# Kernel optimization log

Measured on AMD Instinct MI355X. Metric: run time of the kernel, lower is better.

The kernel has to match this reference:

```python
import jax, jax.numpy as jnp
from jax import lax
import numpy as np

B, H, W = 2048, 28, 28
LATENT_EACH = 64
LATENT = 2 * LATENT_EACH  # 128
MEM_SIZE = 8192
TOPK = 10
EPS = 1e-12


def _conv(x, w, b):
    # x: NCHW, w: OIHW, 3x3 conv, padding=1 (SAME)
    y = lax.conv_general_dilated(x, w, (1, 1), 'SAME',
                                 dimension_numbers=('NCHW', 'OIHW', 'NCHW'))
    return y + b[None, :, None, None]


def _deconv(x, w, b):
    # ConvTranspose2d(k=4, stride=2, padding=1) -> out = 2*in (SAME transpose)
    # w: HWIO = (4,4,in,out)
    y = lax.conv_transpose(x, w, (2, 2), 'SAME',
                           dimension_numbers=('NCHW', 'HWIO', 'NCHW'))
    return y + b[None, :, None, None]


def _encoder(x, w1, b1, w2, b2, fcw, fcb):
    h = jax.nn.relu(_conv(x, w1, b1))
    h = jax.nn.relu(_conv(h, w2, b2))
    feat = h.mean(axis=(2, 3))  # AdaptiveAvgPool2d((1,1)) + flatten -> [B,64]
    return feat @ fcw.T + fcb


def _memory_match(z, mem):
    mn = mem / jnp.maximum(jnp.linalg.norm(mem, axis=1, keepdims=True), EPS)
    zn = z / jnp.maximum(jnp.linalg.norm(z, axis=1, keepdims=True), EPS)
    sim = zn @ mn.T                      # [B, MEM_SIZE]
    topv, topi = lax.top_k(sim, TOPK)    # [B, K]
    wts = jax.nn.softmax(topv, axis=1)   # [B, K]
    sel = mem[topi]                      # gather: [B, K, LATENT]
    return jnp.einsum('bk,bkd->bd', wts, sel)


def setup_inputs() -> dict:
    key = jax.random.key(0)
    ks = jax.random.split(key, 24)
    g = lambda k, s, scale=0.05: jax.random.normal(k, s, jnp.float32) * scale
    inp = {
        'x': jax.random.normal(ks[0], (B, 1, H, W), jnp.float32),
        # center encoder
        'ce_w1': g(ks[1], (32, 1, 3, 3)), 'ce_b1': jnp.zeros((32,), jnp.float32),
        'ce_w2': g(ks[2], (64, 32, 3, 3)), 'ce_b2': jnp.zeros((64,), jnp.float32),
        'ce_fcw': g(ks[3], (LATENT_EACH, 64)), 'ce_fcb': jnp.zeros((LATENT_EACH,), jnp.float32),
        # global encoder
        'ge_w1': g(ks[4], (32, 1, 3, 3)), 'ge_b1': jnp.zeros((32,), jnp.float32),
        'ge_w2': g(ks[5], (64, 32, 3, 3)), 'ge_b2': jnp.zeros((64,), jnp.float32),
        'ge_fcw': g(ks[6], (LATENT_EACH, 64)), 'ge_fcb': jnp.zeros((LATENT_EACH,), jnp.float32),
        # memory bank (Parameter ~ randn)
        'mem': jax.random.normal(ks[7], (MEM_SIZE, LATENT), jnp.float32),
        # decoder
        'dec_fcw': g(ks[8], (64 * 7 * 7, LATENT)), 'dec_fcb': jnp.zeros((64 * 7 * 7,), jnp.float32),
        'd_w1': g(ks[9], (4, 4, 64, 32)), 'd_b1': jnp.zeros((32,), jnp.float32),   # deconv 64->32
        'd_w2': g(ks[10], (16, 32, 3, 3)), 'd_b2': jnp.zeros((16,), jnp.float32),  # conv 32->16
        'd_w3': g(ks[11], (4, 4, 16, 8)), 'd_b3': jnp.zeros((8,), jnp.float32),    # deconv 16->8
        'd_w4': g(ks[12], (1, 8, 3, 3)), 'd_b4': jnp.zeros((1,), jnp.float32),     # conv 8->1
    }
    return inp


def reference(x, ce_w1, ce_b1, ce_w2, ce_b2, ce_fcw, ce_fcb,
              ge_w1, ge_b1, ge_w2, ge_b2, ge_fcw, ge_fcb,
              mem, dec_fcw, dec_fcb,
              d_w1, d_b1, d_w2, d_b2, d_w3, d_b3, d_w4, d_b4):
    # crop_center(x, 14): start = (28-14)//2 = 7
    x_center = x[:, :, 7:21, 7:21]
    z_center = _encoder(x_center, ce_w1, ce_b1, ce_w2, ce_b2, ce_fcw, ce_fcb)
    z_global = _encoder(x, ge_w1, ge_b1, ge_w2, ge_b2, ge_fcw, ge_fcb)
    z = jnp.concatenate([z_center, z_global], axis=1)  # [B, 128]
    z_match = _memory_match(z, mem)                    # [B, 128]
    d = (z_match @ dec_fcw.T + dec_fcb).reshape(B, 64, 7, 7)
    d = jax.nn.relu(_deconv(d, d_w1, d_b1))   # [B,32,14,14]
    d = jax.nn.relu(_conv(d, d_w2, d_b2))     # [B,16,14,14]
    d = jax.nn.relu(_deconv(d, d_w3, d_b3))   # [B,8,28,28]
    x_hat = _conv(d, d_w4, d_b4)              # [B,1,28,28]
    return x_hat
```

## Files before the change

kernel.cpp:

```cpp
#include <hip/hip_runtime.h>
#include <cfloat>
#include <cmath>

#define TPB 256

typedef _Float16 half8 __attribute__((ext_vector_type(8)));
typedef float floatx16 __attribute__((ext_vector_type(16)));
typedef float floatx4 __attribute__((ext_vector_type(4)));

__device__ __forceinline__ float wave_reduce_sum(float v) {
#pragma unroll
  for (int off = 32; off > 0; off >>= 1) v += __shfl_xor(v, off, 64);
  return v;
}

__global__ __launch_bounds__(64) void prep_bfrags(
    const float* __restrict__ ce_w2, const float* __restrict__ ge_w2,
    float* __restrict__ frags) {
  const int blk = blockIdx.x;
  const int enc = blk / 72;
  const int frag = blk % 72;
  const int ks = frag >> 2, part = (frag >> 1) & 1, nt = frag & 1;
  const int tap = ks >> 1, half = ks & 1;
  const int lane = threadIdx.x;
  const float* w2 = enc ? ge_w2 : ce_w2;
  const int n = nt * 32 + (lane & 31);
  const int cb = half * 16 + (lane >> 5) * 8;
  half8 out;
#pragma unroll
  for (int j = 0; j < 8; ++j) {
    float v = w2[(n * 32 + cb + j) * 9 + tap];
    _Float16 h = (_Float16)v;
    out[j] = (part == 0) ? h : (_Float16)((v - (float)h) * 4096.f);
  }
  *(half8*)((char*)frags + ((size_t)blk * 64 + lane) * 16) = out;
}

__global__ __launch_bounds__(64) void prep_dec1(
    const float* __restrict__ w1, float* __restrict__ frags) {
  const int blk = blockIdx.x;
  const int phase = blk >> 4, ks = blk & 15;
  const int pa = phase >> 1, pb = phase & 1;
  const int st = ks >> 2, kk = ks & 3;
  const int s = st >> 1, tt = st & 1;
  const int lane = threadIdx.x;
  const int kg = lane >> 5, n = lane & 31;
  const int tap = (pa + 2 * s) * 4 + (pb + 2 * tt);
  half8 o;
#pragma unroll
  for (int j = 0; j < 8; ++j) {
    int c = kk * 16 + kg * 8 + j;
    o[j] = (_Float16)w1[tap * 2048 + c * 32 + n];
  }
  *(half8*)((char*)frags + ((size_t)blk * 64 + lane) * 16) = o;
}

__global__ __launch_bounds__(64) void prep_dfc(
    const float* __restrict__ dfcw, float* __restrict__ frags) {
  const int blk = blockIdx.x;
  const int nt = blk >> 3, ks = blk & 7;
  const int lane = threadIdx.x;
  const int n = lane & 31, kg = lane >> 5;
  const int j = nt * 32 + n;
  const int px = j >> 6, c = j & 63;
  half8 o;
#pragma unroll
  for (int u = 0; u < 8; ++u)
    o[u] = (_Float16)dfcw[(size_t)(c * 49 + px) * 128 + ks * 16 + kg * 8 + u];
  *(half8*)((char*)frags + ((size_t)blk * 64 + lane) * 16) = o;
}

__global__ __launch_bounds__(64) void prep_mem(
    const float* __restrict__ memg, float* __restrict__ frags) {
  const int blk = blockIdx.x;
  const int slot = blk & 15;
  const int p = slot >> 3, ks = slot & 7;
  const int T = blk >> 4;
  const int lane = threadIdx.x;
  const int n = lane & 31, kg = lane >> 5;
  const float* src = memg + (size_t)(T * 32 + n) * 128 + ks * 16 + kg * 8;
  half8 o;
#pragma unroll
  for (int j = 0; j < 8; ++j) {
    float v = src[j];
    _Float16 h = (_Float16)v;
    o[j] = p ? (_Float16)((v - (float)h) * 4096.f) : h;
  }
  *(half8*)((char*)frags + ((size_t)blk * 64 + lane) * 16) = o;
}

__global__ __launch_bounds__(256) void norm_kernel(
    const float* __restrict__ memg, float* __restrict__ invn) {
  const int wv = threadIdx.x >> 6, lane = threadIdx.x & 63;
  const int row = blockIdx.x * 4 + wv;
  const float* r = memg + (size_t)row * 128;
  float a = r[lane], b = r[lane + 64];
  float s = wave_reduce_sum(a * a + b * b);
  if (lane == 0) invn[row] = 1.f / fmaxf(sqrtf(s), 1e-12f);
}

template <int S, bool CENTER>
__device__ __forceinline__ void encoder_body(
    char* smem, const float* __restrict__ x, const float* __restrict__ w1,
    const float* __restrict__ b1, const float* __restrict__ b2,
    const float* __restrict__ fcw, const float* __restrict__ fcb,
    const float* __restrict__ bfrag, float* __restrict__ zout, int zoff,
    int b) {
  constexpr int SP = S + 2;
  constexpr int NBANDS = (S == 28) ? 3 : 2;
  constexpr int RMAX = 12;
  constexpr int NPIX = RMAX * SP;
  constexpr int GSTB = NPIX * 16;
  constexpr int PSTB = 4 * GSTB;

  char* h1s = smem;
  float* xs = (float*)(smem + 2 * PSTB);
  float* w1s = xs + SP * SP;
  float(*featp)[64] = (float(*)[64])(w1s + 288);

  const int t = threadIdx.x;
  const int lane = t & 63;
  const int wv = t >> 6;

  for (int e = t; e < SP * SP; e += TPB) xs[e] = 0.f;
  for (int e = t; e < 288; e += TPB) w1s[e] = w1[e];
  __syncthreads();
  const float* xb = x + (size_t)b * 784 + (CENTER ? (7 * 28 + 7) : 0);
  for (int e = t; e < S * S; e += TPB) {
    int i = e / S, j = e - i * S;
    xs[(i + 1) * SP + (j + 1)] = xb[i * 28 + j];
  }

  float sp0 = 0.f, sp1 = 0.f;
  const float bias0 = b2[lane & 31];
  const float bias1 = b2[32 + (lane & 31)];
  const int gOff = (lane >> 5) * GSTB;
  const char* bgbase = (const char*)bfrag + lane * 16;

#pragma unroll
  for (int band = 0; band < NBANDS; ++band) {
    const int BH_ = (S == 28) ? ((band < 2) ? 10 : 8) : ((band == 0) ? 10 : 4);
    const int b0 = band * 10;
    const int LIMIT = BH_ * S;
    const int MTB = (LIMIT + 31) / 32;
    const int NBLK2 = (MTB + 1) / 2;

    __syncthreads();
    for (int e = t; e < 4 * NPIX; e += TPB) {
      int g = e / NPIX;
      int pix = e - g * NPIX;
      int lr = pix / SP;
      int cw = pix - lr * SP;
      int gr = b0 - 1 + lr;
      int ebase = g * GSTB + pix * 16;
      half8 hi8 = {}, lo8 = {};
      if (gr >= 0 && gr < S && cw >= 1 && cw <= S) {
        float xv[9];
#pragma unroll
        for (int di = 0; di < 3; ++di)
#pragma unroll
          for (int dj = 0; dj < 3; ++dj)
            xv[di * 3 + dj] = xs[(gr + di) * SP + (cw - 1 + dj)];
#pragma unroll
        for (int u = 0; u < 8; ++u) {
          int ch = g * 8 + u;
          float a = b1[ch];
#pragma unroll
          for (int v = 0; v < 9; ++v) a += xv[v] * w1s[ch * 9 + v];
          a = fmaxf(a, 0.f);
          _Float16 h = (_Float16)a;
          hi8[u] = h;
          lo8[u] = (_Float16)((a - (float)h) * 4096.f);
        }
      }
      *(half8*)(h1s + ebase) = hi8;
      *(half8*)(h1s + PSTB + ebase) = lo8;
    }
    __syncthreads();
    for (int mblk = wv; mblk < NBLK2; mblk += 4) {
      const int Mt0 = mblk * 2;
      floatx16 acc[2][2][2] = {};
      int pixB[2];
#pragma unroll
      for (int im = 0; im < 2; ++im) {
        int px = (Mt0 + im) * 32 + (lane & 31);
        px = px < LIMIT ? px : LIMIT - 1;
        int r = px / S;
        int cc = px - r * S;
        pixB[im] = (r * SP + cc) * 16;
      }
#pragma unroll 3
      for (int tap = 0; tap < 9; ++tap) {
        const int di = tap / 3, dj = tap - di * 3;
        const int offT = (di * SP + dj) * 16;
#pragma unroll
        for (int half = 0; half < 2; ++half) {
          const int ks = tap * 2 + half;
          const char* bp = bgbase + ks * 4096;
          const int offA = offT + gOff + half * (2 * GSTB);
          half8 ah0 = *(const half8*)(h1s + pixB[0] + offA);
          half8 al0 = *(const half8*)(h1s + PSTB + pixB[0] + offA);
          half8 ah1 = *(const half8*)(h1s + pixB[1] + offA);
          half8 al1 = *(const half8*)(h1s + PSTB + pixB[1] + offA);
          {
            half8 bh = *(const half8*)(bp);
            half8 bl = *(const half8*)(bp + 2048);
            acc[0][0][0] = __builtin_amdgcn_mfma_f32_32x32x16_f16(
                ah0, bh, acc[0][0][0], 0, 0, 0);
            acc[0][0][1] = __builtin_amdgcn_mfma_f32_32x32x16_f16(
                ah0, bl, acc[0][0][1], 0, 0, 0);
            acc[0][0][1] = __builtin_amdgcn_mfma_f32_32x32x16_f16(
                al0, bh, acc[0][0][1], 0, 0, 0);
            acc[1][0][0] = __builtin_amdgcn_mfma_f32_32x32x16_f16(
                ah1, bh, acc[1][0][0], 0, 0, 0);
            acc[1][0][1] = __builtin_amdgcn_mfma_f32_32x32x16_f16(
                ah1, bl, acc[1][0][1], 0, 0, 0);
            acc[1][0][1] = __builtin_amdgcn_mfma_f32_32x32x16_f16(
                al1, bh, acc[1][0][1], 0, 0, 0);
          }
          {
            half8 bh = *(const half8*)(bp + 1024);
            half8 bl = *(const half8*)(bp + 3072);
            acc[0][1][0] = __builtin_amdgcn_mfma_f32_32x32x16_f16(
                ah0, bh, acc[0][1][0], 0, 0, 0);
            acc[0][1][1] = __builtin_amdgcn_mfma_f32_32x32x16_f16(
                ah0, bl, acc[0][1][1], 0, 0, 0);
            acc[0][1][1] = __builtin_amdgcn_mfma_f32_32x32x16_f16(
                al0, bh, acc[0][1][1], 0, 0, 0);
            acc[1][1][0] = __builtin_amdgcn_mfma_f32_32x32x16_f16(
                ah1, bh, acc[1][1][0], 0, 0, 0);
            acc[1][1][1] = __builtin_amdgcn_mfma_f32_32x32x16_f16(
                ah1, bl, acc[1][1][1], 0, 0, 0);
            acc[1][1][1] = __builtin_amdgcn_mfma_f32_32x32x16_f16(
                al1, bh, acc[1][1][1], 0, 0, 0);
          }
        }
      }
#pragma unroll
      for (int im = 0; im < 2; ++im)
#pragma unroll
        for (int reg = 0; reg < 16; ++reg) {
          int row = (reg & 3) + 8 * (reg >> 2) + 4 * (lane >> 5);
          int p = (Mt0 + im) * 32 + row;
          if (p < LIMIT) {
            float v0 =
                acc[im][0][0][reg] + acc[im][0][1][reg] * (1.f / 4096.f) + bias0;
            float v1 =
                acc[im][1][0][reg] + acc[im][1][1][reg] * (1.f / 4096.f) + bias1;
            sp0 += fmaxf(v0, 0.f);
            sp1 += fmaxf(v1, 0.f);
          }
        }
    }
  }
  sp0 += __shfl_xor(sp0, 32);
  sp1 += __shfl_xor(sp1, 32);
  if (lane < 32) {
    featp[wv][lane] = sp0;
    featp[wv][32 + lane] = sp1;
  }
  __syncthreads();
  if (t < 64)
    featp[0][t] = (featp[0][t] + featp[1][t] + featp[2][t] + featp[3][t]) *
                  (1.f / (S * S));
  __syncthreads();
  if (t < 64) {
    float s = 0.f;
#pragma unroll
    for (int i = 0; i < 64; ++i) s += featp[0][i] * fcw[t * 64 + i];
    zout[(size_t)b * 128 + zoff + t] = s + fcb[t];
  }
}

__global__ __launch_bounds__(256, 3) void encoders_fused(
    const float* __restrict__ x, const float* __restrict__ ce_w1,
    const float* __restrict__ ce_b1, const float* __restrict__ ce_b2,
    const float* __restrict__ ce_fcw, const float* __restrict__ ce_fcb,
    const float* __restrict__ ge_w1, const float* __restrict__ ge_b1,
    const float* __restrict__ ge_b2, const float* __restrict__ ge_fcw,
    const float* __restrict__ ge_fcb, const float* __restrict__ frags,
    float* __restrict__ z) {
  __shared__ __align__(16) char smem[51856];
  if (blockIdx.x < 2048)
    encoder_body<28, false>(smem, x, ge_w1, ge_b1, ge_b2, ge_fcw, ge_fcb,
                            frags + 18432, z, 64, blockIdx.x);
  else
    encoder_body<14, true>(smem, x, ce_w1, ce_b1, ce_b2, ce_fcw, ce_fcb, frags,
                           z, 0, blockIdx.x - 2048);
}

__global__ __launch_bounds__(256) void match_mfma(
    const float* __restrict__ z, const float* __restrict__ memfrags,
    const float* __restrict__ invn, float* __restrict__ topvw,
    int* __restrict__ topiw) {
  __shared__ __align__(16) char smem[49408];
  float* zs = (float*)smem;
  float* qv = (float*)smem;
  int* qi = (int*)(smem + 16384);
  char* zfrag = smem + 32768;
  float* rowmin = (float*)(smem + 49152);
  int* qn = (int*)(smem + 49152 + 128);

  const int t = threadIdx.x;
  const int lane = t & 63;
  const int wv = t >> 6;
  const int rowbase = blockIdx.x * 32;
  const int Tbase = blockIdx.y * 16;

  for (int e = t; e < 4096; e += TPB) zs[e] = z[(size_t)rowbase * 128 + e];
  if (t < 32) { rowmin[t] = -FLT_MAX; qn[t] = 0; }
  __syncthreads();
#pragma unroll
  for (int h = 0; h < 8; ++h) {
    int r = wv * 8 + h;
    float a = zs[r * 128 + lane], b = zs[r * 128 + 64 + lane];
    float s = wave_reduce_sum(a * a + b * b);
    float inv = 1.f / fmaxf(sqrtf(s), 1e-12f);
    zs[r * 128 + lane] = a * inv;
    zs[r * 128 + 64 + lane] = b * inv;
  }
  __syncthreads();
  for (int e = t; e < 4096; e += TPB) {
    int m = e >> 7, c = e & 127;
    float v = zs[m * 128 + c];
    _Float16 h = (_Float16)v;
    _Float16 l = (_Float16)((v - (float)h) * 4096.f);
    int ks = c >> 4, kg = (c >> 3) & 1, j = c & 7;
    int off = (ks * 64 + kg * 32 + m) * 16 + j * 2;
    *(_Float16*)(zfrag + off) = h;
    *(_Float16*)(zfrag + 8192 + off) = l;
  }
  __syncthreads();

  half8 ah[8], al[8];
  {
    const char* zf = zfrag + ((lane >> 5) * 32 + (lane & 31)) * 16;
#pragma unroll
    for (int ks = 0; ks < 8; ++ks) {
      ah[ks] = *(const half8*)(zf + ks * 1024);
      al[ks] = *(const half8*)(zf + 8192 + ks * 1024);
    }
  }

  float av[10];
  int ai[10];
#pragma unroll
  for (int i = 0; i < 10; ++i) { av[i] = -FLT_MAX; ai[i] = 0; }

#pragma unroll 1
  for (int round = 0; round < 4; ++round) {
    const int T = Tbase + round * 4 + wv;
    const char* bf = (const char*)memfrags + (size_t)T * 16384 + lane * 16;
    floatx16 acc0 = {}, acc1 = {};
#pragma unroll
    for (int ks = 0; ks < 8; ++ks) {
      half8 bh = *(const half8*)(bf + ks * 1024);
      half8 bl = *(const half8*)(bf + 8192 + ks * 1024);
      acc0 = __builtin_amdgcn_mfma_f32_32x32x16_f16(ah[ks], bh, acc0, 0, 0, 0);
      acc1 = __builtin_amdgcn_mfma_f32_32x32x16_f16(ah[ks], bl, acc1, 0, 0, 0);
      acc1 = __builtin_amdgcn_mfma_f32_32x32x16_f16(al[ks], bh, acc1, 0, 0, 0);
    }
    const int gn = T * 32 + (lane & 31);
    const float iv = invn[gn];
#pragma unroll
    for (int reg = 0; reg < 16; ++reg) {
      int m = (reg & 3) + 8 * (reg >> 2) + 4 * (lane >> 5);
      float v = (acc0[reg] + acc1[reg] * (1.f / 4096.f)) * iv;
      if (v > rowmin[m]) {
        int k = atomicAdd(&qn[m], 1);
        qv[m * 128 + k] = v;
        qi[m * 128 + k] = gn;
      }
    }
    __syncthreads();
    if (t < 32) {
      int n = qn[t];
      for (int k = 0; k < n; ++k) {
        float v = qv[t * 128 + k];
        int mm = qi[t * 128 + k];
        if (v > av[9]) {
#pragma unroll
          for (int i = 0; i < 10; ++i) {
            if (v > av[i]) {
              float tv = av[i]; av[i] = v; v = tv;
              int ti = ai[i]; ai[i] = mm; mm = ti;
            }
          }
        }
      }
      qn[t] = 0;
      rowmin[t] = av[9];
    }
    __syncthreads();
  }

  if (t < 32) {
    const size_t base = (size_t)(rowbase + t) * 160 + blockIdx.y * 10;
#pragma unroll
    for (int k = 0; k < 10; ++k) {
      topvw[base + k] = av[k];
      topiw[base + k] = ai[k];
    }
  }
}

__global__ __launch_bounds__(256) void match_merge(
    const float* __restrict__ topvw, const int* __restrict__ topiw,
    const float* __restrict__ memg, _Float16* __restrict__ zmf16) {
  __shared__ float topw[8][10];
  __shared__ int topidx[8][10];
  const int t = threadIdx.x;
  const int rowbase = blockIdx.x * 8;

  if (t < 8) {
    float av[10];
    int ai[10];
#pragma unroll
    for (int i = 0; i < 10; ++i) { av[i] = -FLT_MAX; ai[i] = 0; }
    const size_t base = (size_t)(rowbase + t) * 160;
    for (int c = 0; c < 160; ++c) {
      float v = topvw[base + c];
      int m = topiw[base + c];
      if (v > av[9]) {
#pragma unroll
        for (int i = 0; i < 10; ++i) {
          if (v > av[i]) {
            float tv = av[i]; av[i] = v; v = tv;
            int ti = ai[i]; ai[i] = m; m = ti;
          }
        }
      }
    }
    float e_[10], s = 0.f;
#pragma unroll
    for (int k = 0; k < 10; ++k) { e_[k] = expf(av[k]); s += e_[k]; }
    float inv = 1.f / s;
#pragma unroll
    for (int k = 0; k < 10; ++k) { topw[t][k] = e_[k] * inv; topidx[t][k] = ai[k]; }
  }
  __syncthreads();
  for (int e = t; e < 8 * 128; e += TPB) {
    int r = e >> 7, d = e & 127;
    float o = 0.f;
#pragma unroll
    for (int k = 0; k < 10; ++k)
      o += topw[r][k] * memg[(size_t)topidx[r][k] * 128 + d];
    zmf16[(size_t)(rowbase + r) * 128 + d] = (_Float16)o;
  }
}

__global__ __launch_bounds__(256) void decfc_kernel(
    const _Float16* __restrict__ zmf16, const float* __restrict__ fcb,
    const float* __restrict__ dfcfrags, _Float16* __restrict__ d0f16) {
  const int t = threadIdx.x;
  const int lane = t & 63;
  const int wv = t >> 6;
  const int r0 = blockIdx.x * 32;
  const int ntbase = blockIdx.y * 49;

  half8 a[8];
  {
    const _Float16* ap =
        zmf16 + (size_t)(r0 + (lane & 31)) * 128 + (lane >> 5) * 8;
#pragma unroll
    for (int ks = 0; ks < 8; ++ks) a[ks] = *(const half8*)(ap + ks * 16);
  }
  const char* fb = (const char*)dfcfrags + lane * 16;

  for (int nt = ntbase + wv; nt < ntbase + 49; nt += 4) {
    half8 bfr[8];
    const char* p = fb + (size_t)nt * 8192;
#pragma unroll
    for (int ks = 0; ks < 8; ++ks) bfr[ks] = *(const half8*)(p + ks * 1024);
    floatx16 acc = {};
#pragma unroll
    for (int ks = 0; ks < 8; ++ks)
      acc = __builtin_amdgcn_mfma_f32_32x32x16_f16(a[ks], bfr[ks], acc, 0, 0, 0);
    const int col = nt * 32 + (lane & 31);
    const int px = col >> 6, c = col & 63;
    const float bias = fcb[c * 49 + px];
#pragma unroll
    for (int reg = 0; reg < 16; ++reg) {
      int row = (reg & 3) + 8 * (reg >> 2) + 4 * (lane >> 5);
      d0f16[((size_t)(r0 + row) * 49 + px) * 64 + c] = (_Float16)(acc[reg] + bias);
    }
  }
}

__global__ __launch_bounds__(256) void decoder_kernel(
    const _Float16* __restrict__ d0f16, const float* __restrict__ b1,
    const float* __restrict__ w2, const float* __restrict__ b2,
    const float* __restrict__ w3, const float* __restrict__ b3,
    const float* __restrict__ w4, const float* __restrict__ b4,
    const float* __restrict__ dec1frags, float* __restrict__ out) {
  __shared__ __align__(16) char dsm[41408];
  char* d0f = dsm;
  float* d2 = (float*)dsm;
  char* d1f = dsm + 12608;
  char* w2s = dsm + 28992;
  float* d3 = (float*)(dsm + 12608);

  const int b = blockIdx.x;
  const int t = threadIdx.x;
  const int lane = t & 63;
  const int wv = t >> 6;

  for (int e = t; e < 648; e += TPB) {
    int g = e / 81, pix = e - g * 81;
    int ih = pix / 9 - 1, iw = pix % 9 - 1;
    half8 hv = {};
    if (ih >= 0 && ih < 7 && iw >= 0 && iw < 7)
      hv = *(const half8*)(d0f16 + ((size_t)b * 49 + ih * 7 + iw) * 64 + g * 8);
    *(half8*)(d0f + e * 16) = hv;
  }
  for (int e = t; e < 576; e += TPB) {
    int tau = e / 64, l = e - tau * 64;
    int n = l & 15, kq = l >> 4;
    half8 v;
#pragma unroll
    for (int u = 0; u < 8; ++u)
      v[u] = (_Float16)w2[(n * 32 + kq * 8 + u) * 9 + tau];
    *(half8*)(w2s + e * 16) = v;
  }
  for (int e = t; e < 1024; e += TPB)
    *(float4*)(d1f + e * 16) = make_float4(0.f, 0.f, 0.f, 0.f);
  __syncthreads();

  {
    const int pa = wv >> 1, pb = wv & 1;
    const int kg = lane >> 5, o = lane & 31;
    const char* bg = (const char*)dec1frags + wv * 16384 + lane * 16;
    int pxa[2][4];
#pragma unroll
    for (int im = 0; im < 2; ++im) {
      int px = im * 32 + o;
      px = px < 49 ? px : 48;
      int i = px / 7, j2 = px - i * 7;
#pragma unroll
      for (int st = 0; st < 4; ++st) {
        int s = st >> 1, tt = st & 1;
        pxa[im][st] = ((i + pa + s) * 9 + (j2 + pb + tt)) * 16;
      }
    }
    floatx16 acc0 = {}, acc1 = {};
    half8 nb = *(const half8*)(bg);
#pragma unroll
    for (int ks = 0; ks < 16; ++ks) {
      half8 bf = nb;
      if (ks < 15) nb = *(const half8*)(bg + (ks + 1) * 1024);
      const int gbase = (((ks & 3) * 2 + kg) * 81) * 16;
      half8 a0 = *(const half8*)(d0f + gbase + pxa[0][ks >> 2]);
      half8 a1 = *(const half8*)(d0f + gbase + pxa[1][ks >> 2]);
      acc0 = __builtin_amdgcn_mfma_f32_32x32x16_f16(a0, bf, acc0, 0, 0, 0);
      acc1 = __builtin_amdgcn_mfma_f32_32x32x16_f16(a1, bf, acc1, 0, 0, 0);
    }
    const float bias = b1[o];
    char* dst = d1f + (o >> 3) * 4096 + (o & 7) * 2;
#pragma unroll
    for (int im = 0; im < 2; ++im) {
      const floatx16& ac = im ? acc1 : acc0;
#pragma unroll
      for (int reg = 0; reg < 16; ++reg) {
        int row = (reg & 3) + 8 * (reg >> 2) + 4 * kg;
        int px = im * 32 + row;
        if (px < 49) {
          int i = px / 7, j2 = px - i * 7;
          int p = 2 * i + pa, q = 2 * j2 + pb;
          *(_Float16*)(dst + ((p + 1) * 16 + (q + 1)) * 16) =
              (_Float16)fmaxf(ac[reg] + bias, 0.f);
        }
      }
    }
  }
  __syncthreads();

  {
    const int m = lane & 15, kq = lane >> 4;
    half8 bq[9];
#pragma unroll
    for (int tau = 0; tau < 9; ++tau)
      bq[tau] = *(const half8*)(w2s + (tau * 64 + lane) * 16);
    for (int mt = wv; mt < 13; mt += 4) {
      int px = mt * 16 + m;
      px = px < 196 ? px : 195;
      const int p = px / 14, q = px - (px / 14) * 14;
      floatx4 acc = {};
#pragma unroll
      for (int tau = 0; tau < 9; ++tau) {
        const int dp = tau / 3, dq = tau - dp * 3;
        half8 av =
            *(const half8*)(d1f + (kq * 256 + (p + dp) * 16 + (q + dq)) * 16);
        acc = __builtin_amdgcn_mfma_f32_16x16x32_f16(av, bq[tau], acc, 0, 0, 0);
      }
      const int o = lane & 15;
      const float bias = b2[o];
#pragma unroll
      for (int reg = 0; reg < 4; ++reg) {
        int row = (lane >> 4) * 4 + reg;
        int opx = mt * 16 + row;
        if (opx < 196) d2[o * 197 + opx] = fmaxf(acc[reg] + bias, 0.f);
      }
    }
  }
  __syncthreads();
  for (int e = t; e < 7200; e += TPB) d3[e] = 0.f;
  __syncthreads();

  {
    const int ph = __builtin_amdgcn_readfirstlane(t >> 6);
    const int pa = ph >> 1, pb = ph & 1;
    const int tb = pa * 4 + pb;
    const float* wA = w3 + (size_t)tb * 128;
    const float* wB = w3 + (size_t)(tb + 2) * 128;
    const float* wC = w3 + (size_t)(tb + 8) * 128;
    const float* wD = w3 + (size_t)(tb + 10) * 128;
#pragma unroll 1
    for (int k = 0; k < 4; ++k) {
      const int px = lane + 64 * k;
      const int cpx = px < 196 ? px : 195;
      const int i = cpx / 14, j = cpx % 14;
      int ih[2], iw[2];
      float mh[2], mw[2];
#pragma unroll
      for (int s = 0; s < 2; ++s) {
        int v = i + pa + s - 1;
        mh[s] = (v >= 0 && v <= 13) ? 1.f : 0.f;
        ih[s] = v < 0 ? 0 : (v > 13 ? 13 : v);
        int u = j + pb + s - 1;
        mw[s] = (u >= 0 && u <= 13) ? 1.f : 0.f;
        iw[s] = u < 0 ? 0 : (u > 13 ? 13 : u);
      }
      const float m00 = mh[0] * mw[0], m01 = mh[0] * mw[1];
      const float m10 = mh[1] * mw[0], m11 = mh[1] * mw[1];
      float acc[8];
#pragma unroll
      for (int oo = 0; oo < 8; ++oo) acc[oo] = b3[oo];
#pragma unroll 2
      for (int c = 0; c < 16; ++c) {
        const float a00 = d2[c * 197 + ih[0] * 14 + iw[0]] * m00;
        const float a01 = d2[c * 197 + ih[0] * 14 + iw[1]] * m01;
        const float a10 = d2[c * 197 + ih[1] * 14 + iw[0]] * m10;
        const float a11 = d2[c * 197 + ih[1] * 14 + iw[1]] * m11;
        const int wb = c * 8;
#pragma unroll
        for (int oo = 0; oo < 8; ++oo)
          acc[oo] += a00 * wA[wb + oo] + a01 * wB[wb + oo] +
                     a10 * wC[wb + oo] + a11 * wD[wb + oo];
      }
      if (px < 196) {
        const int p = 2 * i + pa, q = 2 * j + pb;
        const int widx = (p + 1) * 30 + (q + 1);
#pragma unroll
        for (int oo = 0; oo < 8; ++oo)
          d3[oo * 900 + widx] = fmaxf(acc[oo], 0.f);
      }
    }
  }
  __syncthreads();

  for (int e = t; e < 784; e += TPB) {
    int p = e / 28, q = e - p * 28;
    float a = b4[0];
#pragma unroll
    for (int c = 0; c < 8; ++c) {
      const float* bp = &d3[c * 900 + p * 30 + q];
#pragma unroll
      for (int di = 0; di < 3; ++di)
#pragma unroll
        for (int dj = 0; dj < 3; ++dj)
          a += bp[di * 30 + dj] * w4[c * 9 + di * 3 + dj];
    }
    out[(size_t)b * 784 + e] = a;
  }
}

extern "C" void kernel_launch(void* const* d_in, const int* in_sizes, int n_in,
                              void* d_out, int out_size, void* d_ws,
                              size_t ws_size, hipStream_t stream) {
  const float* x      = (const float*)d_in[0];
  const float* ce_w1  = (const float*)d_in[1];
  const float* ce_b1  = (const float*)d_in[2];
  const float* ce_w2  = (const float*)d_in[3];
  const float* ce_b2  = (const float*)d_in[4];
  const float* ce_fcw = (const float*)d_in[5];
  const float* ce_fcb = (const float*)d_in[6];
  const float* ge_w1  = (const float*)d_in[7];
  const float* ge_b1  = (const float*)d_in[8];
  const float* ge_w2  = (const float*)d_in[9];
  const float* ge_b2  = (const float*)d_in[10];
  const float* ge_fcw = (const float*)d_in[11];
  const float* ge_fcb = (const float*)d_in[12];
  const float* memg   = (const float*)d_in[13];
  const float* dfcw   = (const float*)d_in[14];
  const float* dfcb   = (const float*)d_in[15];
  const float* d_w1   = (const float*)d_in[16];
  const float* d_b1   = (const float*)d_in[17];
  const float* d_w2   = (const float*)d_in[18];
  const float* d_b2   = (const float*)d_in[19];
  const float* d_w3   = (const float*)d_in[20];
  const float* d_b3   = (const float*)d_in[21];
  const float* d_w4   = (const float*)d_in[22];
  const float* d_b4   = (const float*)d_in[23];
  float* outp = (float*)d_out;

  float*     ws        = (float*)d_ws;
  float*     z         = ws;
  _Float16*  zmf16     = (_Float16*)(ws + 262144);
  float*     invn      = ws + 262144 + 131072;
  float*     frags     = invn + 8192;
  float*     dec1frags = frags + 36864;
  float*     dfcfrags  = dec1frags + 16384;
  float*     memfrags  = dfcfrags + 200704;
  float*     tailbase  = memfrags + 1048576;
  float*     topvw     = tailbase;
  int*       topiw     = (int*)(tailbase + 327680);
  _Float16*  d0f16     = (_Float16*)tailbase;

  prep_bfrags<<<144, 64, 0, stream>>>(ce_w2, ge_w2, frags);
  prep_dec1<<<64, 64, 0, stream>>>(d_w1, dec1frags);
  prep_dfc<<<784, 64, 0, stream>>>(dfcw, dfcfrags);
  prep_mem<<<4096, 64, 0, stream>>>(memg, memfrags);
  norm_kernel<<<2048, TPB, 0, stream>>>(memg, invn);
  encoders_fused<<<4096, TPB, 0, stream>>>(x, ce_w1, ce_b1, ce_b2, ce_fcw,
                                           ce_fcb, ge_w1, ge_b1, ge_b2, ge_fcw,
                                           ge_fcb, frags, z);
  match_mfma<<<dim3(64, 16), TPB, 0, stream>>>(z, memfrags, invn, topvw, topiw);
  match_merge<<<256, TPB, 0, stream>>>(topvw, topiw, memg, zmf16);
  decfc_kernel<<<dim3(64, 2), TPB, 0, stream>>>(zmf16, dfcb, dfcfrags, d0f16);
  decoder_kernel<<<2048, TPB, 0, stream>>>(d0f16, d_b1, d_w2, d_b2, d_w3, d_b3,
                                           d_w4, d_b4, dec1frags, outp);
}
```

Before: 658.6 us.

## Rebalance encoder conv2 MFMA work per wave and keep conv1 weights in registers

The second encoder conv now gives each wave single units of one 32-pixel M tile by one 32-channel N half, replacing the old blocks of two M tiles by both N halves. This evens out the work across the four waves and cuts accumulator registers. The cost is that A fragments are read from LDS twice, once per N half. Conv1 now has each wave compute one 8-channel group, with its weights and biases held in registers as float2 pairs so the compiler can use packed FMAs. This removes the LDS weight staging and its per-pixel loads. The feature reduction is changed to match the new per-wave channel split.

```diff
diff --git a/kernel.cpp b/kernel.cpp
--- a/kernel.cpp
+++ b/kernel.cpp
@@ -7,6 +7,7 @@
 typedef _Float16 half8 __attribute__((ext_vector_type(8)));
 typedef float floatx16 __attribute__((ext_vector_type(16)));
 typedef float floatx4 __attribute__((ext_vector_type(4)));
+typedef float floatx2 __attribute__((ext_vector_type(2)));
 
 __device__ __forceinline__ float wave_reduce_sum(float v) {
 #pragma unroll
@@ -115,15 +116,28 @@
 
   char* h1s = smem;
   float* xs = (float*)(smem + 2 * PSTB);
-  float* w1s = xs + SP * SP;
-  float(*featp)[64] = (float(*)[64])(w1s + 288);
+  float* featp = xs + SP * SP;
 
   const int t = threadIdx.x;
   const int lane = t & 63;
   const int wv = t >> 6;
+  const int ntW = wv & 1;
+
+  const int gbase = __builtin_amdgcn_readfirstlane(wv * 8);
+  floatx2 w1p[4][9];
+  floatx2 b1p[4];
+#pragma unroll
+  for (int up = 0; up < 4; ++up) {
+    b1p[up][0] = b1[gbase + 2 * up];
+    b1p[up][1] = b1[gbase + 2 * up + 1];
+#pragma unroll
+    for (int v = 0; v < 9; ++v) {
+      w1p[up][v][0] = w1[(gbase + 2 * up) * 9 + v];
+      w1p[up][v][1] = w1[(gbase + 2 * up + 1) * 9 + v];
+    }
+  }
 
   for (int e = t; e < SP * SP; e += TPB) xs[e] = 0.f;
-  for (int e = t; e < 288; e += TPB) w1s[e] = w1[e];
   __syncthreads();
   const float* xb = x + (size_t)b * 784 + (CENTER ? (7 * 28 + 7) : 0);
   for (int e = t; e < S * S; e += TPB) {
@@ -131,9 +145,8 @@
     xs[(i + 1) * SP + (j + 1)] = xb[i * 28 + j];
   }
 
-  float sp0 = 0.f, sp1 = 0.f;
-  const float bias0 = b2[lane & 31];
-  const float bias1 = b2[32 + (lane & 31)];
+  float sp = 0.f;
+  const float biasW = b2[ntW * 32 + (lane & 31)];
   const int gOff = (lane >> 5) * GSTB;
   const char* bgbase = (const char*)bfrag + lane * 16;
 
@@ -143,16 +156,11 @@
     const int b0 = band * 10;
     const int LIMIT = BH_ * S;
     const int MTB = (LIMIT + 31) / 32;
-    const int NBLK2 = (MTB + 1) / 2;
 
     __syncthreads();
-    for (int e = t; e < 4 * NPIX; e += TPB) {
-      int g = e / NPIX;
-      int pix = e - g * NPIX;
-      int lr = pix / SP;
-      int cw = pix - lr * SP;
+    for (int pix = lane; pix < NPIX; pix += 64) {
+      int lr = pix / SP, cw = pix - lr * SP;
       int gr = b0 - 1 + lr;
-      int ebase = g * GSTB + pix * 16;
       half8 hi8 = {}, lo8 = {};
       if (gr >= 0 && gr < S && cw >= 1 && cw <= S) {
         float xv[9];
@@ -162,112 +170,68 @@
           for (int dj = 0; dj < 3; ++dj)
             xv[di * 3 + dj] = xs[(gr + di) * SP + (cw - 1 + dj)];
 #pragma unroll
-        for (int u = 0; u < 8; ++u) {
-          int ch = g * 8 + u;
-          float a = b1[ch];
-#pragma unroll
-          for (int v = 0; v < 9; ++v) a += xv[v] * w1s[ch * 9 + v];
-          a = fmaxf(a, 0.f);
-          _Float16 h = (_Float16)a;
-          hi8[u] = h;
-          lo8[u] = (_Float16)((a - (float)h) * 4096.f);
+        for (int up = 0; up < 4; ++up) {
+          floatx2 a2 = b1p[up];
+#pragma unroll
+          for (int v = 0; v < 9; ++v) a2 += xv[v] * w1p[up][v];
+#pragma unroll
+          for (int q = 0; q < 2; ++q) {
+            float a = fmaxf(a2[q], 0.f);
+            _Float16 h = (_Float16)a;
+            hi8[2 * up + q] = h;
+            lo8[2 * up + q] = (_Float16)((a - (float)h) * 4096.f);
+          }
         }
       }
+      const int ebase = wv * GSTB + pix * 16;
       *(half8*)(h1s + ebase) = hi8;
       *(half8*)(h1s + PSTB + ebase) = lo8;
     }
     __syncthreads();
-    for (int mblk = wv; mblk < NBLK2; mblk += 4) {
-      const int Mt0 = mblk * 2;
-      floatx16 acc[2][2][2] = {};
-      int pixB[2];
-#pragma unroll
-      for (int im = 0; im < 2; ++im) {
-        int px = (Mt0 + im) * 32 + (lane & 31);
-        px = px < LIMIT ? px : LIMIT - 1;
-        int r = px / S;
-        int cc = px - r * S;
-        pixB[im] = (r * SP + cc) * 16;
-      }
-#pragma unroll 3
+#pragma unroll 1
+    for (int u = wv; u < 2 * MTB; u += 4) {
+      const int mt = u >> 1;
+      floatx16 accH = {}, accL = {};
+      int px = mt * 32 + (lane & 31);
+      px = px < LIMIT ? px : LIMIT - 1;
+      const int r = px / S, cc = px - r * S;
+      const int pixB = (r * SP + cc) * 16;
+#pragma unroll
       for (int tap = 0; tap < 9; ++tap) {
         const int di = tap / 3, dj = tap - di * 3;
         const int offT = (di * SP + dj) * 16;
 #pragma unroll
         for (int half = 0; half < 2; ++half) {
           const int ks = tap * 2 + half;
-          const char* bp = bgbase + ks * 4096;
-          const int offA = offT + gOff + half * (2 * GSTB);
-          half8 ah0 = *(const half8*)(h1s + pixB[0] + offA);
-          half8 al0 = *(const half8*)(h1s + PSTB + pixB[0] + offA);
-          half8 ah1 = *(const half8*)(h1s + pixB[1] + offA);
-          half8 al1 = *(const half8*)(h1s + PSTB + pixB[1] + offA);
-          {
-            half8 bh = *(const half8*)(bp);
-            half8 bl = *(const half8*)(bp + 2048);
-            acc[0][0][0] = __builtin_amdgcn_mfma_f32_32x32x16_f16(
-                ah0, bh, acc[0][0][0], 0, 0, 0);
-            acc[0][0][1] = __builtin_amdgcn_mfma_f32_32x32x16_f16(
-                ah0, bl, acc[0][0][1], 0, 0, 0);
-            acc[0][0][1] = __builtin_amdgcn_mfma_f32_32x32x16_f16(
-                al0, bh, acc[0][0][1], 0, 0, 0);
-            acc[1][0][0] = __builtin_amdgcn_mfma_f32_32x32x16_f16(
-                ah1, bh, acc[1][0][0], 0, 0, 0);
-            acc[1][0][1] = __builtin_amdgcn_mfma_f32_32x32x16_f16(
-                ah1, bl, acc[1][0][1], 0, 0, 0);
-            acc[1][0][1] = __builtin_amdgcn_mfma_f32_32x32x16_f16(
-                al1, bh, acc[1][0][1], 0, 0, 0);
-          }
-          {
-            half8 bh = *(const half8*)(bp + 1024);
-            half8 bl = *(const half8*)(bp + 3072);
-            acc[0][1][0] = __builtin_amdgcn_mfma_f32_32x32x16_f16(
-                ah0, bh, acc[0][1][0], 0, 0, 0);
-            acc[0][1][1] = __builtin_amdgcn_mfma_f32_32x32x16_f16(
-                ah0, bl, acc[0][1][1], 0, 0, 0);
-            acc[0][1][1] = __builtin_amdgcn_mfma_f32_32x32x16_f16(
-                al0, bh, acc[0][1][1], 0, 0, 0);
-            acc[1][1][0] = __builtin_amdgcn_mfma_f32_32x32x16_f16(
-                ah1, bh, acc[1][1][0], 0, 0, 0);
-            acc[1][1][1] = __builtin_amdgcn_mfma_f32_32x32x16_f16(
-                ah1, bl, acc[1][1][1], 0, 0, 0);
-            acc[1][1][1] = __builtin_amdgcn_mfma_f32_32x32x16_f16(
-                al1, bh, acc[1][1][1], 0, 0, 0);
-          }
+          const char* bp = bgbase + ks * 4096 + ntW * 1024;
+          const int offA = pixB + offT + gOff + half * (2 * GSTB);
+          half8 ah = *(const half8*)(h1s + offA);
+          half8 al = *(const half8*)(h1s + PSTB + offA);
+          half8 bh = *(const half8*)(bp);
+          half8 bl = *(const half8*)(bp + 2048);
+          accH = __builtin_amdgcn_mfma_f32_32x32x16_f16(ah, bh, accH, 0, 0, 0);
+          accL = __builtin_amdgcn_mfma_f32_32x32x16_f16(ah, bl, accL, 0, 0, 0);
+          accL = __builtin_amdgcn_mfma_f32_32x32x16_f16(al, bh, accL, 0, 0, 0);
         }
       }
 #pragma unroll
-      for (int im = 0; im < 2; ++im)
-#pragma unroll
-        for (int reg = 0; reg < 16; ++reg) {
-          int row = (reg & 3) + 8 * (reg >> 2) + 4 * (lane >> 5);
-          int p = (Mt0 + im) * 32 + row;
-          if (p < LIMIT) {
-            float v0 =
-                acc[im][0][0][reg] + acc[im][0][1][reg] * (1.f / 4096.f) + bias0;
-            float v1 =
-                acc[im][1][0][reg] + acc[im][1][1][reg] * (1.f / 4096.f) + bias1;
-            sp0 += fmaxf(v0, 0.f);
-            sp1 += fmaxf(v1, 0.f);
-          }
-        }
-    }
-  }
-  sp0 += __shfl_xor(sp0, 32);
-  sp1 += __shfl_xor(sp1, 32);
-  if (lane < 32) {
-    featp[wv][lane] = sp0;
-    featp[wv][32 + lane] = sp1;
-  }
-  __syncthreads();
-  if (t < 64)
-    featp[0][t] = (featp[0][t] + featp[1][t] + featp[2][t] + featp[3][t]) *
-                  (1.f / (S * S));
+      for (int reg = 0; reg < 16; ++reg) {
+        int row = (reg & 3) + 8 * (reg >> 2) + 4 * (lane >> 5);
+        int p = mt * 32 + row;
+        if (p < LIMIT)
+          sp += fmaxf(accH[reg] + accL[reg] * (1.f / 4096.f) + biasW, 0.f);
+      }
+    }
+  }
+  sp += __shfl_xor(sp, 32);
+  if (lane < 32) featp[wv * 32 + lane] = sp;
+  __syncthreads();
+  if (t < 64) featp[t] = (featp[t] + featp[64 + t]) * (1.f / (S * S));
   __syncthreads();
   if (t < 64) {
     float s = 0.f;
 #pragma unroll
-    for (int i = 0; i < 64; ++i) s += featp[0][i] * fcw[t * 64 + i];
+    for (int i = 0; i < 64; ++i) s += featp[i] * fcw[t * 64 + i];
     zout[(size_t)b * 128 + zoff + t] = s + fcb[t];
   }
 }
@@ -280,7 +244,7 @@
     const float* __restrict__ ge_b2, const float* __restrict__ ge_fcw,
     const float* __restrict__ ge_fcb, const float* __restrict__ frags,
     float* __restrict__ z) {
-  __shared__ __align__(16) char smem[51856];
+  __shared__ __align__(16) char smem[50192];
   if (blockIdx.x < 2048)
     encoder_body<28, false>(smem, x, ge_w1, ge_b1, ge_b2, ge_fcw, ge_fcb,
                             frags + 18432, z, 64, blockIdx.x);
```

After: 723.3 us. 1.1x slower.
